# Performance work log

Hardware: AMD Instinct MI355X
Metric: run time of the kernel (lower is better)

## Reference

```python
import jax, jax.numpy as jnp
import numpy as np

B, L, D = 4, 2048, 2048
H = 16
DH = D // H           # 128
DC = 512              # d_kv_compress


def rotate_half(x):
    x1, x2 = jnp.split(x, 2, axis=-1)
    return jnp.concatenate([-x2, x1], axis=-1)


def apply_rotary_emb(x, cos, sin):
    return x * cos + rotate_half(x) * sin


def setup_inputs() -> dict:
    key = jax.random.key(0)
    ks = jax.random.split(key, 8)
    s = 1.0 / np.sqrt(D)
    sc = 1.0 / np.sqrt(DC)
    return {
        "x": jax.random.normal(ks[0], (B, L, D), jnp.float32),
        "rope_cos": jax.random.uniform(ks[1], (B, L, DH), jnp.float32),
        "rope_sin": jax.random.uniform(ks[2], (B, L, DH), jnp.float32),
        # weights stored as (out, in) like nn.Linear
        "W_q": jax.random.normal(ks[3], (D, D), jnp.float32) * s,
        "W_dkv": jax.random.normal(ks[4], (DC, D), jnp.float32) * s,
        "W_uk": jax.random.normal(ks[5], (D, DC), jnp.float32) * sc,
        "W_uv": jax.random.normal(ks[6], (D, DC), jnp.float32) * sc,
        "W_o": jax.random.normal(ks[7], (D, D), jnp.float32) * s,
    }


def reference(x, rope_cos, rope_sin, W_q, W_dkv, W_uk, W_uv, W_o):
    scale = DH ** (-0.5)
    # projections: y = x @ W.T
    Q = (x @ W_q.T).reshape(B, L, H, DH).transpose(0, 2, 1, 3)    # [B,H,L,DH]
    c_kv = x @ W_dkv.T                                            # [B,L,DC]
    K = (c_kv @ W_uk.T).reshape(B, L, H, DH).transpose(0, 2, 1, 3)
    V = (c_kv @ W_uv.T).reshape(B, L, H, DH).transpose(0, 2, 1, 3)
    cos = rope_cos[:, None, :, :]  # [B,1,L,DH]
    sin = rope_sin[:, None, :, :]
    Q = apply_rotary_emb(Q, cos, sin)
    K = apply_rotary_emb(K, cos, sin)
    # non-causal SDPA
    scores = jnp.einsum("bhqd,bhkd->bhqk", Q, K) * scale
    attn = jax.nn.softmax(scores, axis=-1)
    out = jnp.einsum("bhqk,bhkd->bhqd", attn, V)                  # [B,H,L,DH]
    out = out.transpose(0, 2, 1, 3).reshape(B, L, D)
    return out @ W_o.T
```

## Files before the change

### kernel.cpp

```cpp
#include <hip/hip_runtime.h>
#include <math.h>

typedef __attribute__((ext_vector_type(8))) short bf16x8;
typedef __attribute__((ext_vector_type(4))) float f32x4;
typedef __attribute__((ext_vector_type(16))) float f32x16;

#define NB 4
#define NL 2048
#define ND 2048
#define NH 16
#define NDH 128
#define NDC 512
#define NROWS (NB*NL)

__device__ __forceinline__ unsigned short f2bf(float f) {
  unsigned int u = __float_as_uint(f);
  u += 0x7fffu + ((u >> 16) & 1u);
  return (unsigned short)(u >> 16);
}
__device__ __forceinline__ float bf2f(unsigned short h) {
  return __uint_as_float(((unsigned int)h) << 16);
}
__device__ __forceinline__ unsigned int pack2bf(float a, float b) {
  return (unsigned int)f2bf(a) | ((unsigned int)f2bf(b) << 16);
}

__device__ __forceinline__ void gld16(const void* g, void* l) {
  __builtin_amdgcn_global_load_lds((const __attribute__((address_space(1))) void*)g,
                                   (__attribute__((address_space(3))) void*)l, 16, 0, 0);
}

__global__ void cvt_kernel(const float4* __restrict__ in, ushort4* __restrict__ out, int n4) {
  int stride = gridDim.x * blockDim.x;
  for (int i = blockIdx.x * blockDim.x + threadIdx.x; i < n4; i += stride) {
    float4 v = in[i];
    ushort4 o;
    o.x = f2bf(v.x); o.y = f2bf(v.y); o.z = f2bf(v.z); o.w = f2bf(v.w);
    out[i] = o;
  }
}

template<int OUT_F32>
__global__ __launch_bounds__(256) void gemm_nt(const unsigned short* __restrict__ A,
                                               const unsigned short* __restrict__ Bm,
                                               void* __restrict__ Cv,
                                               int M, int N, int K) {
  __shared__ unsigned short As[128 * 32];
  __shared__ unsigned short Bs[128 * 32];
  const int tid = threadIdx.x;
  const int wid = tid >> 6;
  const int lane = tid & 63;
  const int wr = wid >> 1, wc = wid & 1;
  const long bm = blockIdx.y, bn = blockIdx.x;
  const int r15 = lane & 15;
  const int koff = (lane >> 4) * 8;
  const int srow = lane >> 2;
  const int scol = (lane & 3) * 8;

  f32x4 acc[4][4];
#pragma unroll
  for (int m = 0; m < 4; ++m)
#pragma unroll
    for (int n = 0; n < 4; ++n) acc[m][n] = (f32x4){0.f, 0.f, 0.f, 0.f};

  const unsigned short* Ablk = A + (bm * 128 + wid * 16 + srow) * (long)K + scol;
  const unsigned short* Bblk = Bm + (bn * 128 + wid * 16 + srow) * (long)K + scol;
  unsigned short* AsW = As + wid * 16 * 32;
  unsigned short* BsW = Bs + wid * 16 * 32;

  for (int kk = 0; kk < K; kk += 32) {
    __syncthreads();
#pragma unroll
    for (int j = 0; j < 2; ++j) {
      gld16(Ablk + (long)j * 64 * K + kk, AsW + j * 64 * 32);
      gld16(Bblk + (long)j * 64 * K + kk, BsW + j * 64 * 32);
    }
    __syncthreads();
    bf16x8 af[4], bfr[4];
#pragma unroll
    for (int m = 0; m < 4; ++m)
      af[m] = *(const bf16x8*)(As + (wr * 64 + m * 16 + r15) * 32 + koff);
#pragma unroll
    for (int n = 0; n < 4; ++n)
      bfr[n] = *(const bf16x8*)(Bs + (wc * 64 + n * 16 + r15) * 32 + koff);
#pragma unroll
    for (int m = 0; m < 4; ++m)
#pragma unroll
      for (int n = 0; n < 4; ++n)
        acc[m][n] = __builtin_amdgcn_mfma_f32_16x16x32_bf16(af[m], bfr[n], acc[m][n], 0, 0, 0);
  }

  const int rr = (lane >> 4) * 4;
#pragma unroll
  for (int m = 0; m < 4; ++m) {
#pragma unroll
    for (int n = 0; n < 4; ++n) {
      long row0 = bm * 128 + wr * 64 + m * 16 + rr;
      long col = bn * 128 + wc * 64 + n * 16 + r15;
#pragma unroll
      for (int r = 0; r < 4; ++r) {
        float v = acc[m][n][r];
        if (OUT_F32) ((float*)Cv)[(row0 + r) * (long)N + col] = v;
        else ((unsigned short*)Cv)[(row0 + r) * (long)N + col] = f2bf(v);
      }
    }
  }
}

template<int OUT_F32>
__global__ __launch_bounds__(512) void gemm_nt256(const unsigned short* __restrict__ A,
                                                  const unsigned short* __restrict__ Bm,
                                                  void* __restrict__ Cv,
                                                  int M, int N, int K) {
  __shared__ unsigned short lds[2][2][16384];
  const int tid = threadIdx.x;
  const int wid = tid >> 6, lane = tid & 63;
  const int wm = wid >> 2, wn = wid & 3;
  const int r15 = lane & 15, khi = lane >> 4;

  const int gx = gridDim.x;
  int bid = blockIdx.y * gx + blockIdx.x;
  int cpx = (gx * gridDim.y) >> 3;
  int swz = (bid & 7) * cpx + (bid >> 3);
  const long bm = swz / gx, bn = swz % gx;

  const int c0 = tid, c1 = 512 + tid;
  const int r0 = c0 >> 3, r1 = c1 >> 3;
  const int cs0 = ((c0 & 7) ^ (r0 & 7)) * 8;
  const int cs1 = ((c1 & 7) ^ (r1 & 7)) * 8;
  const unsigned short* srcA = A + (bm * 256) * (long)K;
  const unsigned short* srcB = Bm + (bn * 256) * (long)K;

#define STAGE256(mat, h, kb, bufi) do {                                              \
    const unsigned short* s_ = (mat) ? srcB : srcA;                                  \
    gld16(s_ + ((h) * 128 + r0) * (long)K + (kb) + cs0,                              \
          &lds[bufi][mat][(h) * 8192 + wid * 512]);                                  \
    gld16(s_ + ((h) * 128 + r1) * (long)K + (kb) + cs1,                              \
          &lds[bufi][mat][(h) * 8192 + 4096 + wid * 512]);                           \
  } while (0)

  f32x4 acc[8][4];
#pragma unroll
  for (int m = 0; m < 8; ++m)
#pragma unroll
    for (int n = 0; n < 4; ++n) acc[m][n] = (f32x4){0.f, 0.f, 0.f, 0.f};

  const int NT = K >> 6;
  STAGE256(0, 0, 0, 0); STAGE256(0, 1, 0, 0);
  STAGE256(1, 0, 0, 0); STAGE256(1, 1, 0, 0);

  for (int t = 0; t < NT; ++t) {
    const int buf = t & 1, nbuf = buf ^ 1;
    const int kb1 = (t + 1) << 6;
    const bool pf = (t + 1 < NT);
    __builtin_amdgcn_s_barrier();
    if (pf) {
      STAGE256(0, 0, kb1, nbuf);
      asm volatile("s_waitcnt vmcnt(2)" ::: "memory");
    } else {
      asm volatile("s_waitcnt vmcnt(0)" ::: "memory");
    }
    __builtin_amdgcn_s_barrier();

    bf16x8 bfr[4][2];
#pragma unroll
    for (int n = 0; n < 4; ++n)
#pragma unroll
      for (int kk = 0; kk < 2; ++kk) {
        int rb = wn * 64 + n * 16 + r15;
        bfr[n][kk] = *(const bf16x8*)&lds[buf][1][rb * 64 + (((kk * 4 + khi) ^ (rb & 7)) * 8)];
      }
#pragma unroll
    for (int mb = 0; mb < 4; ++mb) {
      if (mb != 0) {
        __builtin_amdgcn_s_barrier();
        if (pf) {
          if (mb == 1) STAGE256(0, 1, kb1, nbuf);
          else if (mb == 2) STAGE256(1, 0, kb1, nbuf);
          else STAGE256(1, 1, kb1, nbuf);
        }
      }
      bf16x8 af[2][2];
#pragma unroll
      for (int m2 = 0; m2 < 2; ++m2)
#pragma unroll
        for (int kk = 0; kk < 2; ++kk) {
          int ra = wm * 128 + mb * 32 + m2 * 16 + r15;
          af[m2][kk] = *(const bf16x8*)&lds[buf][0][ra * 64 + (((kk * 4 + khi) ^ (ra & 7)) * 8)];
        }
      asm volatile("s_waitcnt lgkmcnt(0)" ::: "memory");
      __builtin_amdgcn_sched_barrier(0);
      __builtin_amdgcn_s_setprio(1);
#pragma unroll
      for (int m2 = 0; m2 < 2; ++m2)
#pragma unroll
        for (int n = 0; n < 4; ++n)
#pragma unroll
          for (int kk = 0; kk < 2; ++kk)
            acc[mb * 2 + m2][n] = __builtin_amdgcn_mfma_f32_16x16x32_bf16(
                af[m2][kk], bfr[n][kk], acc[mb * 2 + m2][n], 0, 0, 0);
      __builtin_amdgcn_s_setprio(0);
    }
  }
#undef STAGE256

#pragma unroll
  for (int mi = 0; mi < 8; ++mi) {
#pragma unroll
    for (int n = 0; n < 4; ++n) {
      long row0 = bm * 256 + wm * 128 + mi * 16 + khi * 4;
      long col = bn * 256 + wn * 64 + n * 16 + r15;
#pragma unroll
      for (int r = 0; r < 4; ++r) {
        float v = acc[mi][n][r];
        if (OUT_F32) ((float*)Cv)[(row0 + r) * (long)N + col] = v;
        else ((unsigned short*)Cv)[(row0 + r) * (long)N + col] = f2bf(v);
      }
    }
  }
}

__global__ void rope_kernel(unsigned short* __restrict__ Qb, const float* __restrict__ cosb,
                            const float* __restrict__ sinb, float scale) {
  const long row = blockIdx.x;
  const float* cr = cosb + row * NDH;
  const float* sr = sinb + row * NDH;
  unsigned short* q = Qb + row * (long)ND;
  for (int p = threadIdx.x; p < NH * 64; p += blockDim.x) {
    int h = p >> 6, d = p & 63;
    int i1 = h * 128 + d, i2 = i1 + 64;
    float q1 = bf2f(q[i1]), q2 = bf2f(q[i2]);
    float c1 = cr[d], c2 = cr[d + 64], s1 = sr[d], s2 = sr[d + 64];
    float o1 = (q1 * c1 - q2 * s1) * scale;
    float o2 = (q2 * c2 + q1 * s2) * scale;
    q[i1] = f2bf(o1);
    q[i2] = f2bf(o2);
  }
}

__global__ __launch_bounds__(512) void flash_attn(const unsigned short* __restrict__ Qb,
                                                  const unsigned short* __restrict__ Kb,
                                                  const unsigned short* __restrict__ Vb,
                                                  unsigned short* __restrict__ Ob) {
  __shared__ unsigned short ldsbuf[18432];
  unsigned short* Ks = ldsbuf;
  unsigned short* Vt = ldsbuf + 8192;

  const int tid = threadIdx.x, wid = tid >> 6, lane = tid & 63;
  const int l31 = lane & 31, hi5 = lane >> 5;
  const int bh = blockIdx.y, qt = blockIdx.x;
  const int b = bh >> 4, h = bh & 15;
  const long rowbase = (long)b * NL;
  const int colbase = h * NDH;
  const long q0 = (long)qt * 256 + wid * 32;

  bf16x8 qf[8];
  {
    const unsigned short* qp = Qb + (rowbase + q0 + l31) * (long)ND + colbase + hi5 * 8;
#pragma unroll
    for (int kc = 0; kc < 8; ++kc) qf[kc] = *(const bf16x8*)(qp + kc * 16);
  }

  f32x16 oacc[4];
#pragma unroll
  for (int db = 0; db < 4; ++db)
#pragma unroll
    for (int i = 0; i < 16; ++i) oacc[db][i] = 0.f;
  float mrun = -1e30f, lrun = 0.f;

  const int key0 = tid >> 4;
  const int c8 = (tid & 15) * 8;
  const int ksw = c8 ^ ((key0 & 7) << 3);
  bf16x8 kreg[2], vreg[2];

#pragma unroll
  for (int j = 0; j < 2; ++j) {
    const long grow = (rowbase + key0 + 32 * j) * (long)ND + colbase + c8;
    kreg[j] = *(const bf16x8*)(Kb + grow);
    vreg[j] = *(const bf16x8*)(Vb + grow);
  }

  for (int kt = 0; kt < NL / 64; ++kt) {
    __syncthreads();
#pragma unroll
    for (int j = 0; j < 2; ++j) {
      int key = key0 + 32 * j;
      *(bf16x8*)(Ks + key * 128 + ksw) = kreg[j];
#pragma unroll
      for (int i = 0; i < 8; ++i) {
        int d = c8 + i;
        int kcol = key ^ (((d >> 3) & 7) << 3);
        Vt[d * 72 + kcol] = (unsigned short)vreg[j][i];
      }
    }
    __syncthreads();
    if (kt + 1 < NL / 64) {
#pragma unroll
      for (int j = 0; j < 2; ++j) {
        const long grow = (rowbase + (kt + 1) * 64 + key0 + 32 * j) * (long)ND + colbase + c8;
        kreg[j] = *(const bf16x8*)(Kb + grow);
        vreg[j] = *(const bf16x8*)(Vb + grow);
      }
    }

    f32x16 sacc[2];
#pragma unroll
    for (int nb = 0; nb < 2; ++nb) {
#pragma unroll
      for (int i = 0; i < 16; ++i) sacc[nb][i] = 0.f;
#pragma unroll
      for (int kc = 0; kc < 8; ++kc) {
        int row = nb * 32 + l31;
        bf16x8 kf = *(const bf16x8*)(Ks + row * 128 + ((kc * 16 + hi5 * 8) ^ ((row & 7) << 3)));
        sacc[nb] = __builtin_amdgcn_mfma_f32_32x32x16_bf16(kf, qf[kc], sacc[nb], 0, 0, 0);
      }
    }

    float mx = sacc[0][0];
#pragma unroll
    for (int nb = 0; nb < 2; ++nb)
#pragma unroll
      for (int r = 0; r < 16; ++r) mx = fmaxf(mx, sacc[nb][r]);
    mx = fmaxf(mx, __shfl_xor(mx, 32));
    if (!__all(mx - mrun <= 8.f)) {
      float mnew = fmaxf(mrun, mx);
      float corr = __expf(mrun - mnew);
      mrun = mnew;
      lrun *= corr;
#pragma unroll
      for (int db = 0; db < 4; ++db)
#pragma unroll
        for (int i = 0; i < 16; ++i) oacc[db][i] *= corr;
    }
    float s = 0.f;
#pragma unroll
    for (int nb = 0; nb < 2; ++nb)
#pragma unroll
      for (int r = 0; r < 16; ++r) {
        float e = __expf(sacc[nb][r] - mrun);
        sacc[nb][r] = e;
        s += e;
      }
    s += __shfl_xor(s, 32);
    lrun += s;

    union { unsigned int u[4]; bf16x8 v; } pa[2][2];
#pragma unroll
    for (int nb = 0; nb < 2; ++nb) {
      unsigned int x1 = pack2bf(sacc[nb][0], sacc[nb][1]);
      unsigned int x2 = pack2bf(sacc[nb][2], sacc[nb][3]);
      unsigned int y1 = pack2bf(sacc[nb][4], sacc[nb][5]);
      unsigned int y2 = pack2bf(sacc[nb][6], sacc[nb][7]);
      unsigned int z1 = pack2bf(sacc[nb][8], sacc[nb][9]);
      unsigned int z2 = pack2bf(sacc[nb][10], sacc[nb][11]);
      unsigned int w1 = pack2bf(sacc[nb][12], sacc[nb][13]);
      unsigned int w2 = pack2bf(sacc[nb][14], sacc[nb][15]);
      unsigned int sx1 = __shfl_xor((int)x1, 32), sx2 = __shfl_xor((int)x2, 32);
      unsigned int sy1 = __shfl_xor((int)y1, 32), sy2 = __shfl_xor((int)y2, 32);
      unsigned int sz1 = __shfl_xor((int)z1, 32), sz2 = __shfl_xor((int)z2, 32);
      unsigned int sw1 = __shfl_xor((int)w1, 32), sw2 = __shfl_xor((int)w2, 32);
      pa[nb][0].u[0] = hi5 ? sy1 : x1;
      pa[nb][0].u[1] = hi5 ? sy2 : x2;
      pa[nb][0].u[2] = hi5 ? y1 : sx1;
      pa[nb][0].u[3] = hi5 ? y2 : sx2;
      pa[nb][1].u[0] = hi5 ? sw1 : z1;
      pa[nb][1].u[1] = hi5 ? sw2 : z2;
      pa[nb][1].u[2] = hi5 ? w1 : sz1;
      pa[nb][1].u[3] = hi5 ? w2 : sz2;
    }

#pragma unroll
    for (int db = 0; db < 4; ++db) {
      int d = db * 32 + l31;
      int dsw = ((d >> 3) & 7) << 3;
#pragma unroll
      for (int nb = 0; nb < 2; ++nb)
#pragma unroll
        for (int ks = 0; ks < 2; ++ks) {
          int keybase8 = nb * 32 + ks * 16 + hi5 * 8;
          bf16x8 vf = *(const bf16x8*)(Vt + d * 72 + (keybase8 ^ dsw));
          oacc[db] = __builtin_amdgcn_mfma_f32_32x32x16_bf16(vf, pa[nb][ks].v, oacc[db], 0, 0, 0);
        }
    }
  }

  __syncthreads();
  float rinv = 1.0f / lrun;
  unsigned short* scr = ldsbuf + wid * 2304;
#pragma unroll
  for (int c = 0; c < 2; ++c) {
    asm volatile("s_waitcnt lgkmcnt(0)" ::: "memory");
    __builtin_amdgcn_sched_barrier(0);
#pragma unroll
    for (int dbh = 0; dbh < 2; ++dbh) {
      int db = 2 * c + dbh;
#pragma unroll
      for (int t = 0; t < 8; ++t) {
        int d_lo = dbh * 32 + ((2 * t) & 3) + 8 * (t >> 1) + 4 * hi5;
        unsigned int pv = pack2bf(oacc[db][2 * t] * rinv, oacc[db][2 * t + 1] * rinv);
        *(unsigned int*)(scr + l31 * 72 + d_lo) = pv;
      }
    }
    asm volatile("s_waitcnt lgkmcnt(0)" ::: "memory");
    __builtin_amdgcn_sched_barrier(0);
#pragma unroll
    for (int j = 0; j < 4; ++j) {
      int row = j * 8 + (lane >> 3);
      bf16x8 ov = *(const bf16x8*)(scr + row * 72 + (lane & 7) * 8);
      *(bf16x8*)(Ob + (rowbase + q0 + row) * (long)ND + colbase + c * 64 + (lane & 7) * 8) = ov;
    }
  }
}

extern "C" void kernel_launch(void* const* d_in, const int* in_sizes, int n_in,
                              void* d_out, int out_size, void* d_ws, size_t ws_size,
                              hipStream_t stream) {
  const float* x = (const float*)d_in[0];
  const float* rope_cos = (const float*)d_in[1];
  const float* rope_sin = (const float*)d_in[2];
  const float* W_q = (const float*)d_in[3];
  const float* W_dkv = (const float*)d_in[4];
  const float* W_uk = (const float*)d_in[5];
  const float* W_uv = (const float*)d_in[6];
  const float* W_o = (const float*)d_in[7];
  float* out = (float*)d_out;

  char* p = (char*)d_ws;
  unsigned short* xb = (unsigned short*)p;    p += (size_t)NROWS * ND * 2;
  unsigned short* Wqb = (unsigned short*)p;   p += (size_t)ND * ND * 2;
  unsigned short* Wdkvb = (unsigned short*)p; p += (size_t)NDC * ND * 2;
  unsigned short* Wukb = (unsigned short*)p;  p += (size_t)ND * NDC * 2;
  unsigned short* Wuvb = (unsigned short*)p;  p += (size_t)ND * NDC * 2;
  unsigned short* Wob = (unsigned short*)p;   p += (size_t)ND * ND * 2;
  unsigned short* Qb = (unsigned short*)p;    p += (size_t)NROWS * ND * 2;
  unsigned short* ckv = (unsigned short*)p;   p += (size_t)NROWS * NDC * 2;
  unsigned short* Kbf = (unsigned short*)p;   p += (size_t)NROWS * ND * 2;
  unsigned short* Vbf = (unsigned short*)p;   p += (size_t)NROWS * ND * 2;
  unsigned short* AO = (unsigned short*)p;    p += (size_t)NROWS * ND * 2;

  {
    struct { const float* s; unsigned short* d; long n; } cv[6] = {
      {x, xb, (long)NROWS * ND},
      {W_q, Wqb, (long)ND * ND},
      {W_dkv, Wdkvb, (long)NDC * ND},
      {W_uk, Wukb, (long)ND * NDC},
      {W_uv, Wuvb, (long)ND * NDC},
      {W_o, Wob, (long)ND * ND},
    };
    for (int i = 0; i < 6; ++i) {
      int n4 = (int)(cv[i].n / 4);
      int blocks = (n4 + 255) / 256;
      if (blocks > 2048) blocks = 2048;
      cvt_kernel<<<blocks, 256, 0, stream>>>((const float4*)cv[i].s, (ushort4*)cv[i].d, n4);
    }
  }

  gemm_nt256<0><<<dim3(ND / 256, NROWS / 256), 512, 0, stream>>>(xb, Wqb, Qb, NROWS, ND, ND);
  gemm_nt<0><<<dim3(NDC / 128, NROWS / 128), 256, 0, stream>>>(xb, Wdkvb, ckv, NROWS, NDC, ND);
  gemm_nt256<0><<<dim3(ND / 256, NROWS / 256), 512, 0, stream>>>(ckv, Wukb, Kbf, NROWS, ND, NDC);
  gemm_nt256<0><<<dim3(ND / 256, NROWS / 256), 512, 0, stream>>>(ckv, Wuvb, Vbf, NROWS, ND, NDC);

  const float scale = 0.08838834764831845f;
  rope_kernel<<<NROWS, 256, 0, stream>>>(Qb, rope_cos, rope_sin, scale);
  rope_kernel<<<NROWS, 256, 0, stream>>>(Kbf, rope_cos, rope_sin, 1.0f);

  flash_attn<<<dim3(NL / 256, NB * NH), 512, 0, stream>>>(Qb, Kbf, Vbf, AO);

  gemm_nt256<1><<<dim3(ND / 256, NROWS / 256), 512, 0, stream>>>(AO, Wob, out, NROWS, ND, ND);
}
```

Before: 485.0 us.

## Double-buffer K/V tiles in flash attention, use exp2 with folded log2e, remap blocks

The flash attention kernel now double-buffers the K and transposed V tiles in LDS. The next tile is written after the QK MFMAs and global loads run two tiles ahead, which drops one of the two barriers per iteration. V is stored as packed key pairs in 32-bit words with a new swizzle, exp is replaced by the raw v_exp_f32 (base 2) with log2(e) folded into the Q scale, and the block index is remapped so adjacent blocks share K/V for the same head. This raises LDS use and register pressure (launch bounds now request 4 blocks), which may limit occupancy.

```diff
diff --git a/kernel.cpp b/kernel.cpp
--- a/kernel.cpp
+++ b/kernel.cpp
@@ -23,6 +23,9 @@
 }
 __device__ __forceinline__ unsigned int pack2bf(float a, float b) {
   return (unsigned int)f2bf(a) | ((unsigned int)f2bf(b) << 16);
+}
+__device__ __forceinline__ float exp2_fast(float x) {
+  float r; asm("v_exp_f32 %0, %1" : "=v"(r) : "v"(x)); return r;
 }
 
 __device__ __forceinline__ void gld16(const void* g, void* l) {
@@ -238,17 +241,19 @@
   }
 }
 
-__global__ __launch_bounds__(512) void flash_attn(const unsigned short* __restrict__ Qb,
-                                                  const unsigned short* __restrict__ Kb,
-                                                  const unsigned short* __restrict__ Vb,
-                                                  unsigned short* __restrict__ Ob) {
-  __shared__ unsigned short ldsbuf[18432];
-  unsigned short* Ks = ldsbuf;
-  unsigned short* Vt = ldsbuf + 8192;
+__global__ __launch_bounds__(512, 4) void flash_attn(const unsigned short* __restrict__ Qb,
+                                                     const unsigned short* __restrict__ Kb,
+                                                     const unsigned short* __restrict__ Vb,
+                                                     unsigned short* __restrict__ Ob) {
+  __shared__ unsigned short KsArr[2 * 8192];
+  __shared__ unsigned int VtArr[2 * 4608];
 
   const int tid = threadIdx.x, wid = tid >> 6, lane = tid & 63;
   const int l31 = lane & 31, hi5 = lane >> 5;
-  const int bh = blockIdx.y, qt = blockIdx.x;
+
+  const int L = blockIdx.y * 8 + blockIdx.x;
+  const int bh = ((L >> 6) << 3) | (L & 7);
+  const int qt = (L >> 3) & 7;
   const int b = bh >> 4, h = bh & 15;
   const long rowbase = (long)b * NL;
   const int colbase = h * NDH;
@@ -268,40 +273,39 @@
     for (int i = 0; i < 16; ++i) oacc[db][i] = 0.f;
   float mrun = -1e30f, lrun = 0.f;
 
-  const int key0 = tid >> 4;
+  const int kp = tid >> 4;
   const int c8 = (tid & 15) * 8;
-  const int ksw = c8 ^ ((key0 & 7) << 3);
   bf16x8 kreg[2], vreg[2];
 
-#pragma unroll
-  for (int j = 0; j < 2; ++j) {
-    const long grow = (rowbase + key0 + 32 * j) * (long)ND + colbase + c8;
-    kreg[j] = *(const bf16x8*)(Kb + grow);
-    vreg[j] = *(const bf16x8*)(Vb + grow);
-  }
-
-  for (int kt = 0; kt < NL / 64; ++kt) {
-    __syncthreads();
-#pragma unroll
-    for (int j = 0; j < 2; ++j) {
-      int key = key0 + 32 * j;
-      *(bf16x8*)(Ks + key * 128 + ksw) = kreg[j];
-#pragma unroll
-      for (int i = 0; i < 8; ++i) {
-        int d = c8 + i;
-        int kcol = key ^ (((d >> 3) & 7) << 3);
-        Vt[d * 72 + kcol] = (unsigned short)vreg[j][i];
-      }
-    }
-    __syncthreads();
-    if (kt + 1 < NL / 64) {
-#pragma unroll
-      for (int j = 0; j < 2; ++j) {
-        const long grow = (rowbase + (kt + 1) * 64 + key0 + 32 * j) * (long)ND + colbase + c8;
-        kreg[j] = *(const bf16x8*)(Kb + grow);
-        vreg[j] = *(const bf16x8*)(Vb + grow);
-      }
-    }
+#define LOAD_KV(kt_) do {                                                          \
+    _Pragma("unroll") for (int j = 0; j < 2; ++j) {                                \
+      const long grow = (rowbase + (kt_) * 64 + 2 * kp + j) * (long)ND + colbase + c8; \
+      kreg[j] = *(const bf16x8*)(Kb + grow);                                       \
+      vreg[j] = *(const bf16x8*)(Vb + grow);                                       \
+    } } while (0)
+
+#define WRITE_KV(bi) do {                                                          \
+    _Pragma("unroll") for (int j = 0; j < 2; ++j) {                                \
+      int row_ = 2 * kp + j;                                                       \
+      *(bf16x8*)(KsArr + (bi) * 8192 + row_ * 128 + (c8 ^ ((row_ & 7) << 3))) = kreg[j]; \
+    }                                                                              \
+    _Pragma("unroll") for (int i = 0; i < 8; ++i) {                                \
+      int d_ = c8 + i;                                                             \
+      VtArr[(bi) * 4608 + d_ * 36 + 4 * ((kp >> 2) ^ ((d_ >> 3) & 7)) + (kp & 3)] = \
+          (unsigned int)(unsigned short)vreg[0][i] |                               \
+          ((unsigned int)(unsigned short)vreg[1][i] << 16);                        \
+    } } while (0)
+
+  LOAD_KV(0);
+  WRITE_KV(0);
+  __syncthreads();
+  LOAD_KV(1);
+
+  const int NT = NL / 64;
+  for (int kt = 0; kt < NT; ++kt) {
+    const int bf = kt & 1;
+    const unsigned short* Ksb = KsArr + bf * 8192;
+    const unsigned int* Vtb = VtArr + bf * 4608;
 
     f32x16 sacc[2];
 #pragma unroll
@@ -311,10 +315,13 @@
 #pragma unroll
       for (int kc = 0; kc < 8; ++kc) {
         int row = nb * 32 + l31;
-        bf16x8 kf = *(const bf16x8*)(Ks + row * 128 + ((kc * 16 + hi5 * 8) ^ ((row & 7) << 3)));
+        bf16x8 kf = *(const bf16x8*)(Ksb + row * 128 + ((kc * 16 + hi5 * 8) ^ ((row & 7) << 3)));
         sacc[nb] = __builtin_amdgcn_mfma_f32_32x32x16_bf16(kf, qf[kc], sacc[nb], 0, 0, 0);
       }
     }
+
+    if (kt + 1 < NT) WRITE_KV(bf ^ 1);
+    if (kt + 2 < NT) LOAD_KV(kt + 2);
 
     float mx = sacc[0][0];
 #pragma unroll
@@ -324,7 +331,7 @@
     mx = fmaxf(mx, __shfl_xor(mx, 32));
     if (!__all(mx - mrun <= 8.f)) {
       float mnew = fmaxf(mrun, mx);
-      float corr = __expf(mrun - mnew);
+      float corr = exp2_fast(mrun - mnew);
       mrun = mnew;
       lrun *= corr;
 #pragma unroll
@@ -337,7 +344,7 @@
     for (int nb = 0; nb < 2; ++nb)
 #pragma unroll
       for (int r = 0; r < 16; ++r) {
-        float e = __expf(sacc[nb][r] - mrun);
+        float e = exp2_fast(sacc[nb][r] - mrun);
         sacc[nb][r] = e;
         s += e;
       }
@@ -372,21 +379,23 @@
 #pragma unroll
     for (int db = 0; db < 4; ++db) {
       int d = db * 32 + l31;
-      int dsw = ((d >> 3) & 7) << 3;
+      int dsw = (d >> 3) & 7;
 #pragma unroll
       for (int nb = 0; nb < 2; ++nb)
 #pragma unroll
         for (int ks = 0; ks < 2; ++ks) {
-          int keybase8 = nb * 32 + ks * 16 + hi5 * 8;
-          bf16x8 vf = *(const bf16x8*)(Vt + d * 72 + (keybase8 ^ dsw));
+          int g = nb * 4 + ks * 2 + hi5;
+          bf16x8 vf = *(const bf16x8*)(Vtb + d * 36 + 4 * (g ^ dsw));
           oacc[db] = __builtin_amdgcn_mfma_f32_32x32x16_bf16(vf, pa[nb][ks].v, oacc[db], 0, 0, 0);
         }
     }
-  }
-
-  __syncthreads();
+    __syncthreads();
+  }
+#undef LOAD_KV
+#undef WRITE_KV
+
   float rinv = 1.0f / lrun;
-  unsigned short* scr = ldsbuf + wid * 2304;
+  unsigned short* scr = (unsigned short*)VtArr + wid * 2304;
 #pragma unroll
   for (int c = 0; c < 2; ++c) {
     asm volatile("s_waitcnt lgkmcnt(0)" ::: "memory");
@@ -460,11 +469,11 @@
   gemm_nt256<0><<<dim3(ND / 256, NROWS / 256), 512, 0, stream>>>(ckv, Wukb, Kbf, NROWS, ND, NDC);
   gemm_nt256<0><<<dim3(ND / 256, NROWS / 256), 512, 0, stream>>>(ckv, Wuvb, Vbf, NROWS, ND, NDC);
 
-  const float scale = 0.08838834764831845f;
-  rope_kernel<<<NROWS, 256, 0, stream>>>(Qb, rope_cos, rope_sin, scale);
+  const float scale_q = 0.08838834764831845f * 1.4426950408889634f;
+  rope_kernel<<<NROWS, 256, 0, stream>>>(Qb, rope_cos, rope_sin, scale_q);
   rope_kernel<<<NROWS, 256, 0, stream>>>(Kbf, rope_cos, rope_sin, 1.0f);
 
-  flash_attn<<<dim3(NL / 256, NB * NH), 512, 0, stream>>>(Qb, Kbf, Vbf, AO);
+  flash_attn<<<dim3(8, NB * NH * 8 / 8), 512, 0, stream>>>(Qb, Kbf, Vbf, AO);
 
   gemm_nt256<1><<<dim3(ND / 256, NROWS / 256), 512, 0, stream>>>(AO, Wob, out, NROWS, ND, ND);
 }
```

Measured after the change: 893.4 us. 1.84x slower.
